# Optimization experiments

Measured on AMD Instinct MI355X. Metric: run time of the kernel, lower is better.

Reference implementation:

```python
import jax, jax.numpy as jnp
import numpy as np

N_HEADS = 32
N_KV_HEADS = 8
HEAD_DIM = 64
D_MODEL = 2048
SLIDING_WINDOW = 512
ROPE_THETA = 10000.0
PAST_LENGTH = 0
EPS = 1e-6


def setup_inputs() -> dict:
    key = jax.random.key(0)
    k1, k2, k3 = jax.random.split(key, 3)
    B, S = 1, 2048
    q_size = N_HEADS * HEAD_DIM
    kv_size = N_KV_HEADS * HEAD_DIM
    return {
        "x": jax.random.normal(k1, (B, S, D_MODEL), dtype=jnp.float32),
        "w_qkv": jax.random.normal(k2, (q_size + 2 * kv_size, D_MODEL), dtype=jnp.float32) * (D_MODEL ** -0.5),
        "w_out": jax.random.normal(k3, (D_MODEL, q_size), dtype=jnp.float32) * (q_size ** -0.5),
        "q_norm_w": jnp.ones((HEAD_DIM,), dtype=jnp.float32),
        "k_norm_w": jnp.ones((HEAD_DIM,), dtype=jnp.float32),
    }


def _rms_norm(x, w):
    xf = x.astype(jnp.float32)
    rms = jax.lax.rsqrt(jnp.mean(xf * xf, axis=-1, keepdims=True) + EPS)
    return (xf * rms).astype(x.dtype) * w


def _rope(q, k, past_length):
    # q: [b, h, s, d], k: [b, kv, s, d]
    s, d = q.shape[2], q.shape[3]
    inv_freq = 1.0 / (ROPE_THETA ** (jnp.arange(0, d, 2, dtype=jnp.float32) / d))
    pos = jnp.arange(s, dtype=jnp.float32) + past_length
    ang = pos[:, None] * inv_freq[None, :]            # [s, d/2]
    emb = jnp.concatenate([ang, ang], axis=-1)        # [s, d]
    cos, sin = jnp.cos(emb), jnp.sin(emb)

    def rot_half(x):
        x1, x2 = jnp.split(x, 2, axis=-1)
        return jnp.concatenate([-x2, x1], axis=-1)

    q = q * cos + rot_half(q) * sin
    k = k * cos + rot_half(k) * sin
    return q, k


def _sliding_mask(seq_len, total_len, past_length):
    q_idx = jnp.arange(seq_len)[:, None]
    k_idx = jnp.arange(total_len)[None, :]
    causal = (q_idx + past_length) >= k_idx
    window = (q_idx + past_length - k_idx) < SLIDING_WINDOW
    keep = causal & window
    return jnp.where(keep, 0.0, -jnp.inf).astype(jnp.float32)[None, None]


def reference(x, w_qkv, w_out, q_norm_w, k_norm_w):
    b, s, _ = x.shape
    n_rep = N_HEADS // N_KV_HEADS
    q_size = N_HEADS * HEAD_DIM
    kv_size = N_KV_HEADS * HEAD_DIM

    qkv = jnp.einsum('bsd,od->bso', x, w_qkv)
    q, k, v = jnp.split(qkv, [q_size, q_size + kv_size], axis=-1)
    q = q.reshape(b, s, N_HEADS, HEAD_DIM).transpose(0, 2, 1, 3)
    k = k.reshape(b, s, N_KV_HEADS, HEAD_DIM).transpose(0, 2, 1, 3)
    v = v.reshape(b, s, N_KV_HEADS, HEAD_DIM).transpose(0, 2, 1, 3)

    q = _rms_norm(q, q_norm_w)
    k = _rms_norm(k, k_norm_w)
    q, k = _rope(q, k, PAST_LENGTH)

    k_rep = jnp.repeat(k, n_rep, axis=1)  # [b, H, s, d]
    v_rep = jnp.repeat(v, n_rep, axis=1)

    scale = HEAD_DIM ** -0.5
    scores = jnp.einsum('bhqd,bhkd->bhqk', q, k_rep) * scale
    scores = scores + _sliding_mask(s, s, PAST_LENGTH)
    probs = jax.nn.softmax(scores, axis=-1)
    attn = jnp.einsum('bhqk,bhkd->bhqd', probs, v_rep)

    attn = attn.transpose(0, 2, 1, 3).reshape(b, s, q_size)
    return jnp.einsum('bso,do->bsd', attn, w_out)
```

## Files before the change

### kernel.cpp

```cpp
#include <hip/hip_runtime.h>

typedef unsigned short u16;
typedef unsigned int u32;
typedef __bf16 bf16x8 __attribute__((ext_vector_type(8)));
typedef float f32x4 __attribute__((ext_vector_type(4)));
typedef float f32x16 __attribute__((ext_vector_type(16)));
typedef u16 u16x8 __attribute__((ext_vector_type(8)));
typedef u32 u32x2 __attribute__((ext_vector_type(2)));

#define MFMA16(a, b, c) __builtin_amdgcn_mfma_f32_16x16x32_bf16((a), (b), (c), 0, 0, 0)
#define MFMA32(a, b, c) __builtin_amdgcn_mfma_f32_32x32x16_bf16((a), (b), (c), 0, 0, 0)

__device__ __forceinline__ u16 f2bf(float f) {
    unsigned int u = __float_as_uint(f);
    u = (u + 0x7FFF + ((u >> 16) & 1)) >> 16;
    return (u16)u;
}

__device__ __forceinline__ u32 cvtpk(float a, float b) {
    u32 d;
    asm("v_cvt_pk_bf16_f32 %0, %1, %2" : "=v"(d) : "v"(a), "v"(b));
    return d;
}

__device__ __forceinline__ void gld_lds16(const u16* g, u16* l) {
    __builtin_amdgcn_global_load_lds(
        (const __attribute__((address_space(1))) unsigned int*)g,
        (__attribute__((address_space(3))) unsigned int*)l, 16, 0, 0);
}

__global__ __launch_bounds__(256) void cvt_bf16(const float* __restrict__ in,
                                                u16* __restrict__ out, int n4) {
    int idx = blockIdx.x * blockDim.x + threadIdx.x;
    int stride = gridDim.x * blockDim.x;
    for (int i = idx; i < n4; i += stride) {
        float4 v = reinterpret_cast<const float4*>(in)[i];
        ushort4 o;
        o.x = f2bf(v.x); o.y = f2bf(v.y); o.z = f2bf(v.z); o.w = f2bf(v.w);
        reinterpret_cast<ushort4*>(out)[i] = o;
    }
}

__global__ __launch_bounds__(256) void reduce_add(const float4* __restrict__ a,
                                                  const float4* __restrict__ b,
                                                  float4* __restrict__ o, int n4) {
    int idx = blockIdx.x * blockDim.x + threadIdx.x;
    int stride = gridDim.x * blockDim.x;
    for (int i = idx; i < n4; i += stride) {
        float4 va = a[i], vb = b[i];
        float4 vo = {va.x + vb.x, va.y + vb.y, va.z + vb.z, va.w + vb.w};
        o[i] = vo;
    }
}

template <int SPLITK>
__global__ __launch_bounds__(256) void gemm_bt(const u16* __restrict__ A,
                                               const u16* __restrict__ B,
                                               float* __restrict__ C,
                                               int M, int N, int K) {
    __shared__ __align__(16) u16 As[2][128 * 32];
    __shared__ __align__(16) u16 Bs[2][128 * 32];

    int nbn = N >> 7;
    int bid = blockIdx.x;
    int nwg = (M >> 7) * nbn;
    int cpx = nwg >> 3;
    int wg = (bid & 7) * cpx + (bid >> 3);
    int tm = wg / nbn, tn = wg % nbn;
    int m0 = tm << 7, n0 = tn << 7;

    int Ks = K / SPLITK;
    int kbase = blockIdx.y * Ks;
    float* Cs = C + (size_t)blockIdx.y * ((size_t)M * N);

    int t = threadIdx.x;
    int w = t >> 6, l = t & 63, lrow = l & 15, lhi = l >> 4;
    int wr = w >> 1, wc = w & 1;

    int e0 = t * 8;
    int row0 = e0 >> 5, col0 = e0 & 31;

    const u16* Ag = A + (size_t)m0 * K + kbase;
    const u16* Bg = B + (size_t)n0 * K + kbase;

    auto stage = [&](int sbuf, int kt) {
        int k0 = kt << 5;
        gld_lds16(Ag + (size_t)row0 * K + k0 + col0, &As[sbuf][e0]);
        gld_lds16(Ag + (size_t)(row0 + 64) * K + k0 + col0, &As[sbuf][e0 + 2048]);
        gld_lds16(Bg + (size_t)row0 * K + k0 + col0, &Bs[sbuf][e0]);
        gld_lds16(Bg + (size_t)(row0 + 64) * K + k0 + col0, &Bs[sbuf][e0 + 2048]);
    };

    f32x4 acc[4][4] = {};
    int NT = Ks >> 5;
    stage(0, 0);
    __syncthreads();
    int buf = 0;
    for (int kt = 0; kt < NT; ++kt) {
        if (kt + 1 < NT) stage(buf ^ 1, kt + 1);
        bf16x8 af[4], bfr[4];
#pragma unroll
        for (int i = 0; i < 4; ++i) {
            af[i]  = *(const bf16x8*)&As[buf][(wr * 64 + i * 16 + lrow) * 32 + lhi * 8];
            bfr[i] = *(const bf16x8*)&Bs[buf][(wc * 64 + i * 16 + lrow) * 32 + lhi * 8];
        }
#pragma unroll
        for (int i = 0; i < 4; ++i)
#pragma unroll
            for (int j = 0; j < 4; ++j)
                acc[i][j] = MFMA16(af[i], bfr[j], acc[i][j]);
        __syncthreads();
        buf ^= 1;
    }
#pragma unroll
    for (int i = 0; i < 4; ++i) {
#pragma unroll
        for (int j = 0; j < 4; ++j) {
            int crow = m0 + wr * 64 + i * 16 + lhi * 4;
            int ccol = n0 + wc * 64 + j * 16 + lrow;
            float* cp = Cs + (size_t)crow * N + ccol;
#pragma unroll
            for (int r2 = 0; r2 < 4; ++r2) cp[(size_t)r2 * N] = acc[i][j][r2];
        }
    }
}

__global__ __launch_bounds__(256) void qkv_post(const float* __restrict__ qkv0,
                                                const float* __restrict__ qkv1,
                                                const float* __restrict__ qw,
                                                const float* __restrict__ kw,
                                                u16* __restrict__ qb,
                                                u16* __restrict__ kb,
                                                u16* __restrict__ vb) {
    int s = blockIdx.x;
    int t = threadIdx.x, w = t >> 6, lane = t & 63;
    const float* row0 = qkv0 + (size_t)s * 3072;
    const float* row1 = qkv1 + (size_t)s * 3072;
    int d2 = lane & 31;
    float inv = exp2f(-(float)d2 * (13.287712379549449f / 32.0f));
    float ang = (float)s * inv;
    float cs = cosf(ang), sn = sinf(ang);
    for (int h = w; h < 48; h += 4) {
        float v = row0[h * 64 + lane] + row1[h * 64 + lane];
        if (h < 40) {
            float ss = v * v;
#pragma unroll
            for (int m = 32; m; m >>= 1) ss += __shfl_xor(ss, m);
            float rms = rsqrtf(ss * (1.0f / 64.0f) + 1e-6f);
            float wgt = (h < 32) ? qw[lane] : kw[lane];
            v = v * rms * wgt;
            float part = __shfl_xor(v, 32);
            float rot = (lane < 32) ? -part : part;
            v = v * cs + rot * sn;
            if (h < 32)
                qb[((size_t)h * 2048 + s) * 64 + lane] = f2bf(v);
            else
                kb[((size_t)(h - 32) * 2048 + s) * 64 + lane] = f2bf(v);
        } else {
            vb[((size_t)(h - 40) * 2048 + s) * 64 + lane] = f2bf(v);
        }
    }
}

__global__ __launch_bounds__(256) void transpose_v(const u16* __restrict__ vb,
                                                   u16* __restrict__ vt) {
    int kv = blockIdx.y;
    int s0 = blockIdx.x * 256;
    __shared__ __align__(16) u16 tile[64][256];
    int t = threadIdx.x;
    int sl = t >> 3;
    int d0 = (t & 7) * 8;
#pragma unroll
    for (int j = 0; j < 8; ++j) {
        int s = sl + j * 32;
        u16x8 v = *(const u16x8*)(vb + ((size_t)kv * 2048 + s0 + s) * 64 + d0);
#pragma unroll
        for (int e = 0; e < 8; ++e) tile[d0 + e][s] = v[e];
    }
    __syncthreads();
    int d = t >> 2;
    int so = (t & 3) * 64;
#pragma unroll
    for (int j = 0; j < 8; ++j) {
        int s_local = so + j * 8;
        *(u16x8*)(vt + ((size_t)kv * 64 + d) * 2048 + s0 + s_local) =
            *(const u16x8*)&tile[d][s_local];
    }
}

__global__ __launch_bounds__(256) void attn_fa2(const u16* __restrict__ qb,
                                                const u16* __restrict__ kb,
                                                const u16* __restrict__ vt,
                                                u16* __restrict__ ab) {
    const float C = 0.18033688011112042f;
    int h = blockIdx.y, kv = h >> 2;
    int t = threadIdx.x, w = t >> 6, l = t & 63;
    int lq = l & 31, hi = l >> 5;
    int qlo = blockIdx.x * 128 + w * 32;
    __shared__ u16 sm[4][32][66];

    const u16* qrow = qb + ((size_t)h * 2048 + qlo + lq) * 64 + hi * 8;
    bf16x8 qf[4];
#pragma unroll
    for (int dk = 0; dk < 4; ++dk) qf[dk] = *(const bf16x8*)(qrow + dk * 16);

    f32x16 oa = {}, ob = {};
    float m = 0.f, lsum = 0.f;

    int kstart = qlo - 511; if (kstart < 0) kstart = 0;
    int kt0 = kstart >> 5, kt1 = qlo >> 5;
    const u16* kb_h = kb + (size_t)kv * 2048 * 64;
    const u16* vt_h = vt + (size_t)kv * 64 * 2048;

    for (int kt = kt0; kt <= kt1; ++kt) {
        int k0 = kt << 5;
        const u16* krow = kb_h + (size_t)(k0 + lq) * 64 + hi * 8;
        bf16x8 kf0 = *(const bf16x8*)(krow);
        bf16x8 kf1 = *(const bf16x8*)(krow + 16);
        bf16x8 kf2 = *(const bf16x8*)(krow + 32);
        bf16x8 kf3 = *(const bf16x8*)(krow + 48);
        const u16* vrow = vt_h + (size_t)lq * 2048 + k0 + hi * 8;
        bf16x8 va0 = *(const bf16x8*)(vrow);
        bf16x8 va1 = *(const bf16x8*)(vrow + 16);
        bf16x8 vb0 = *(const bf16x8*)(vrow + 32 * 2048);
        bf16x8 vb1 = *(const bf16x8*)(vrow + 32 * 2048 + 16);

        f32x16 s = {};
        s = MFMA32(kf0, qf[0], s);
        s = MFMA32(kf1, qf[1], s);
        s = MFMA32(kf2, qf[2], s);
        s = MFMA32(kf3, qf[3], s);

        bool edge = (k0 + 31 > qlo) || (qlo + 31 - k0 >= 512);
        if (edge) {
            int q = qlo + lq;
#pragma unroll
            for (int r = 0; r < 16; ++r) {
                int k = k0 + (r & 3) + 8 * (r >> 2) + 4 * hi;
                if (!((unsigned)(q - k) < 512u)) s[r] = -1e30f;
            }
        }
        float tm = s[0];
#pragma unroll
        for (int r = 1; r < 16; ++r) tm = fmaxf(tm, s[r]);
        tm = fmaxf(tm, __shfl_xor(tm, 32));
        float mnew = fmaxf(m, tm);
        float mc = mnew * C;
        float sf = exp2f(m * C - mc);
        m = mnew;
        float p[16];
        float rs = 0.f;
#pragma unroll
        for (int r = 0; r < 16; ++r) {
            p[r] = exp2f(fmaf(s[r], C, -mc));
            rs += p[r];
        }
        rs += __shfl_xor(rs, 32);
        lsum = lsum * sf + rs;
#pragma unroll
        for (int r = 0; r < 16; ++r) { oa[r] *= sf; ob[r] *= sf; }

        u32 pk0 = cvtpk(p[0], p[1]),   pk1 = cvtpk(p[2], p[3]);
        u32 pk2 = cvtpk(p[4], p[5]),   pk3 = cvtpk(p[6], p[7]);
        u32 pk4 = cvtpk(p[8], p[9]),   pk5 = cvtpk(p[10], p[11]);
        u32 pk6 = cvtpk(p[12], p[13]), pk7 = cvtpk(p[14], p[15]);
        u32x2 r02 = __builtin_amdgcn_permlane32_swap(pk0, pk2, false, false);
        u32x2 r13 = __builtin_amdgcn_permlane32_swap(pk1, pk3, false, false);
        u32x2 r46 = __builtin_amdgcn_permlane32_swap(pk4, pk6, false, false);
        u32x2 r57 = __builtin_amdgcn_permlane32_swap(pk5, pk7, false, false);
        bf16x8 b0, b1;
        {
            u32* bp = (u32*)&b0;
            bp[0] = r02[0]; bp[1] = r13[0]; bp[2] = r02[1]; bp[3] = r13[1];
            u32* bq = (u32*)&b1;
            bq[0] = r46[0]; bq[1] = r57[0]; bq[2] = r46[1]; bq[3] = r57[1];
        }
        oa = MFMA32(va0, b0, oa);
        oa = MFMA32(va1, b1, oa);
        ob = MFMA32(vb0, b0, ob);
        ob = MFMA32(vb1, b1, ob);
    }

    float inv = 1.0f / lsum;
#pragma unroll
    for (int rp = 0; rp < 8; ++rp) {
        int r = rp * 2;
        int d = (r & 3) + 8 * (r >> 2) + 4 * hi;
        *(u32*)&sm[w][lq][d]      = cvtpk(oa[r] * inv, oa[r + 1] * inv);
        *(u32*)&sm[w][lq][d + 32] = cvtpk(ob[r] * inv, ob[r + 1] * inv);
    }
    asm volatile("s_waitcnt lgkmcnt(0)" ::: "memory");
    int qr = l >> 1, dbase = (l & 1) * 32;
    size_t orow = (size_t)(qlo + qr) * 2048 + h * 64 + dbase;
#pragma unroll
    for (int c2 = 0; c2 < 8; ++c2) {
        u32 w0 = *(const u32*)&sm[w][qr][dbase + c2 * 4];
        u32 w1 = *(const u32*)&sm[w][qr][dbase + c2 * 4 + 2];
        u32x2 val = { w0, w1 };
        *(u32x2*)(ab + orow + c2 * 4) = val;
    }
}

extern "C" void kernel_launch(void* const* d_in, const int* in_sizes, int n_in,
                              void* d_out, int out_size, void* d_ws, size_t ws_size,
                              hipStream_t stream) {
    const float* x     = (const float*)d_in[0];
    const float* w_qkv = (const float*)d_in[1];
    const float* w_out = (const float*)d_in[2];
    const float* qw    = (const float*)d_in[3];
    const float* kw    = (const float*)d_in[4];
    float* out = (float*)d_out;

    char* ws = (char*)d_ws;
    u16*   x_b    = (u16*)(ws);
    u16*   wB     = (u16*)(ws + 8388608);
    u16*   q_b    = (u16*)(ws);
    u16*   k_b    = (u16*)(ws + 8388608);
    u16*   v_b    = (u16*)(ws + 10485760);
    u16*   v_t    = (u16*)(ws + 12582912);
    float* P0     = (float*)(ws + 20971520);
    float* O0     = (float*)(ws + 20971520);
    float* O1     = (float*)(ws + 37748736);
    u16*   attn_b = (u16*)(ws + 54525952);

    cvt_bf16<<<2048, 256, 0, stream>>>(x, x_b, 2048 * 2048 / 4);
    cvt_bf16<<<2048, 256, 0, stream>>>(w_qkv, wB, 3072 * 2048 / 4);
    gemm_bt<2><<<dim3(384, 2), 256, 0, stream>>>(x_b, wB, P0, 2048, 3072, 2048);
    qkv_post<<<2048, 256, 0, stream>>>(P0, P0 + (size_t)2048 * 3072, qw, kw, q_b, k_b, v_b);
    transpose_v<<<dim3(8, 8), 256, 0, stream>>>(v_b, v_t);
    attn_fa2<<<dim3(16, 32), 256, 0, stream>>>(q_b, k_b, v_t, attn_b);
    cvt_bf16<<<2048, 256, 0, stream>>>(w_out, wB, 2048 * 2048 / 4);
    gemm_bt<2><<<dim3(256, 2), 256, 0, stream>>>(attn_b, wB, O0, 2048, 2048, 2048);
    reduce_add<<<1024, 256, 0, stream>>>((const float4*)O0, (const float4*)O1,
                                         (float4*)out, 2048 * 2048 / 4);
}
```

Before: 145.6 us.

## Split sliding-window key tiles across waves and merge partial softmax in LDS

Each attention block now handles 32 queries instead of 128. Its four waves take interleaved key tiles of that window, and the grid grows from 512 to 2048 blocks. At the end, each wave writes its unnormalised output, running max and running sum to shared memory. After a barrier the block rescales and merges the four partial softmax states, then writes bf16 output with 16-byte stores. This shortens the serial per-wave loop over key tiles and adds parallelism, at the cost of a block-wide sync, extra fp32 LDS traffic and merge arithmetic. Each block also reloads the Q fragments redundantly.

```diff
diff --git a/kernel.cpp b/kernel.cpp
--- a/kernel.cpp
+++ b/kernel.cpp
@@ -7,6 +7,7 @@
 typedef float f32x16 __attribute__((ext_vector_type(16)));
 typedef u16 u16x8 __attribute__((ext_vector_type(8)));
 typedef u32 u32x2 __attribute__((ext_vector_type(2)));
+typedef u32 u32x4 __attribute__((ext_vector_type(4)));
 
 #define MFMA16(a, b, c) __builtin_amdgcn_mfma_f32_16x16x32_bf16((a), (b), (c), 0, 0, 0)
 #define MFMA32(a, b, c) __builtin_amdgcn_mfma_f32_32x32x16_bf16((a), (b), (c), 0, 0, 0)
@@ -188,7 +189,7 @@
     }
 }
 
-__global__ __launch_bounds__(256) void attn_fa2(const u16* __restrict__ qb,
+__global__ __launch_bounds__(256) void attn_fa3(const u16* __restrict__ qb,
                                                 const u16* __restrict__ kb,
                                                 const u16* __restrict__ vt,
                                                 u16* __restrict__ ab) {
@@ -196,8 +197,9 @@
     int h = blockIdx.y, kv = h >> 2;
     int t = threadIdx.x, w = t >> 6, l = t & 63;
     int lq = l & 31, hi = l >> 5;
-    int qlo = blockIdx.x * 128 + w * 32;
-    __shared__ u16 sm[4][32][66];
+    int qlo = blockIdx.x * 32;
+    __shared__ float Olds[4][64][32];
+    __shared__ float mlds[4][32], llds[4][32];
 
     const u16* qrow = qb + ((size_t)h * 2048 + qlo + lq) * 64 + hi * 8;
     bf16x8 qf[4];
@@ -212,7 +214,7 @@
     const u16* kb_h = kb + (size_t)kv * 2048 * 64;
     const u16* vt_h = vt + (size_t)kv * 64 * 2048;
 
-    for (int kt = kt0; kt <= kt1; ++kt) {
+    for (int kt = kt0 + w; kt <= kt1; kt += 4) {
         int k0 = kt << 5;
         const u16* krow = kb_h + (size_t)(k0 + lq) * 64 + hi * 8;
         bf16x8 kf0 = *(const bf16x8*)(krow);
@@ -281,24 +283,32 @@
         ob = MFMA32(vb1, b1, ob);
     }
 
-    float inv = 1.0f / lsum;
-#pragma unroll
-    for (int rp = 0; rp < 8; ++rp) {
-        int r = rp * 2;
+#pragma unroll
+    for (int r = 0; r < 16; ++r) {
         int d = (r & 3) + 8 * (r >> 2) + 4 * hi;
-        *(u32*)&sm[w][lq][d]      = cvtpk(oa[r] * inv, oa[r + 1] * inv);
-        *(u32*)&sm[w][lq][d + 32] = cvtpk(ob[r] * inv, ob[r + 1] * inv);
-    }
-    asm volatile("s_waitcnt lgkmcnt(0)" ::: "memory");
-    int qr = l >> 1, dbase = (l & 1) * 32;
-    size_t orow = (size_t)(qlo + qr) * 2048 + h * 64 + dbase;
-#pragma unroll
-    for (int c2 = 0; c2 < 8; ++c2) {
-        u32 w0 = *(const u32*)&sm[w][qr][dbase + c2 * 4];
-        u32 w1 = *(const u32*)&sm[w][qr][dbase + c2 * 4 + 2];
-        u32x2 val = { w0, w1 };
-        *(u32x2*)(ab + orow + c2 * 4) = val;
-    }
+        Olds[w][d][lq]      = oa[r];
+        Olds[w][d + 32][lq] = ob[r];
+    }
+    if (hi == 0) { mlds[w][lq] = m; llds[w][lq] = lsum; }
+    __syncthreads();
+
+    int q = t & 31, dg = t >> 5;
+    float m0 = mlds[0][q], m1 = mlds[1][q], m2 = mlds[2][q], m3 = mlds[3][q];
+    float M = fmaxf(fmaxf(m0, m1), fmaxf(m2, m3));
+    float s0 = exp2f((m0 - M) * C), s1 = exp2f((m1 - M) * C);
+    float s2 = exp2f((m2 - M) * C), s3 = exp2f((m3 - M) * C);
+    float lt = llds[0][q] * s0 + llds[1][q] * s1 + llds[2][q] * s2 + llds[3][q] * s3;
+    float inv = 1.0f / lt;
+    float v[8];
+#pragma unroll
+    for (int e = 0; e < 8; ++e) {
+        int d = dg * 8 + e;
+        v[e] = (Olds[0][d][q] * s0 + Olds[1][d][q] * s1 +
+                Olds[2][d][q] * s2 + Olds[3][d][q] * s3) * inv;
+    }
+    u32x4 pkt = { cvtpk(v[0], v[1]), cvtpk(v[2], v[3]),
+                  cvtpk(v[4], v[5]), cvtpk(v[6], v[7]) };
+    *(u32x4*)(ab + (size_t)(qlo + q) * 2048 + h * 64 + dg * 8) = pkt;
 }
 
 extern "C" void kernel_launch(void* const* d_in, const int* in_sizes, int n_in,
@@ -328,7 +338,7 @@
     gemm_bt<2><<<dim3(384, 2), 256, 0, stream>>>(x_b, wB, P0, 2048, 3072, 2048);
     qkv_post<<<2048, 256, 0, stream>>>(P0, P0 + (size_t)2048 * 3072, qw, kw, q_b, k_b, v_b);
     transpose_v<<<dim3(8, 8), 256, 0, stream>>>(v_b, v_t);
-    attn_fa2<<<dim3(16, 32), 256, 0, stream>>>(q_b, k_b, v_t, attn_b);
+    attn_fa3<<<dim3(64, 32), 256, 0, stream>>>(q_b, k_b, v_t, attn_b);
     cvt_bf16<<<2048, 256, 0, stream>>>(w_out, wB, 2048 * 2048 / 4);
     gemm_bt<2><<<dim3(256, 2), 256, 0, stream>>>(attn_b, wB, O0, 2048, 2048, 2048);
     reduce_add<<<1024, 256, 0, stream>>>((const float4*)O0, (const float4*)O1,
```

Measured after the change: 148.0 us. No clear change (+1.6%).

## Triple-buffer GEMM with swizzled LDS; stage K/V in LDS and drop online-softmax max

Applied to the files above, without the earlier changes.

The GEMM moves from double to triple buffering, prefetching three k-tiles ahead with explicit vmcnt waits and barriers. It also XOR-swizzles the LDS tile layout to avoid bank conflicts on the fragment reads. The attention kernel now loads each K/V tile cooperatively into double-buffered, swizzled LDS shared by all four waves, instead of every wave reading global memory. It also folds the softmax scale into Q and drops the running-max rescaling, relying on RMS-normalised Q/K keeping the logits bounded. That last step removes per-tile max/shuffle/rescale work but can overflow if the norm weights are large, and waves with no work still have to join every barrier.

```diff
diff --git a/kernel.cpp b/kernel.cpp
--- a/kernel.cpp
+++ b/kernel.cpp
@@ -7,6 +7,7 @@
 typedef float f32x16 __attribute__((ext_vector_type(16)));
 typedef u16 u16x8 __attribute__((ext_vector_type(8)));
 typedef u32 u32x2 __attribute__((ext_vector_type(2)));
+typedef u32 u32x4 __attribute__((ext_vector_type(4)));
 
 #define MFMA16(a, b, c) __builtin_amdgcn_mfma_f32_16x16x32_bf16((a), (b), (c), 0, 0, 0)
 #define MFMA32(a, b, c) __builtin_amdgcn_mfma_f32_32x32x16_bf16((a), (b), (c), 0, 0, 0)
@@ -58,8 +59,8 @@
                                                const u16* __restrict__ B,
                                                float* __restrict__ C,
                                                int M, int N, int K) {
-    __shared__ __align__(16) u16 As[2][128 * 32];
-    __shared__ __align__(16) u16 Bs[2][128 * 32];
+    __shared__ __align__(16) u16 As[3][128 * 32];
+    __shared__ __align__(16) u16 Bs[3][128 * 32];
 
     int nbn = N >> 7;
     int bid = blockIdx.x;
@@ -78,7 +79,8 @@
     int wr = w >> 1, wc = w & 1;
 
     int e0 = t * 8;
-    int row0 = e0 >> 5, col0 = e0 & 31;
+    int row0 = t >> 2;
+    int col0 = (((t & 3) ^ ((t >> 3) & 3)) << 3);
 
     const u16* Ag = A + (size_t)m0 * K + kbase;
     const u16* Bg = B + (size_t)n0 * K + kbase;
@@ -93,24 +95,38 @@
 
     f32x4 acc[4][4] = {};
     int NT = Ks >> 5;
-    stage(0, 0);
-    __syncthreads();
-    int buf = 0;
+    stage(0, 0); stage(1, 1); stage(2, 2);
+    asm volatile("s_waitcnt vmcnt(8)" ::: "memory");
+    asm volatile("s_barrier" ::: "memory");
+    int cur = 0;
     for (int kt = 0; kt < NT; ++kt) {
-        if (kt + 1 < NT) stage(buf ^ 1, kt + 1);
         bf16x8 af[4], bfr[4];
 #pragma unroll
         for (int i = 0; i < 4; ++i) {
-            af[i]  = *(const bf16x8*)&As[buf][(wr * 64 + i * 16 + lrow) * 32 + lhi * 8];
-            bfr[i] = *(const bf16x8*)&Bs[buf][(wc * 64 + i * 16 + lrow) * 32 + lhi * 8];
-        }
+            int row = wr * 64 + i * 16 + lrow;
+            af[i] = *(const bf16x8*)&As[cur][row * 32 + ((lhi ^ ((row >> 1) & 3)) << 3)];
+        }
+#pragma unroll
+        for (int j = 0; j < 4; ++j) {
+            int row = wc * 64 + j * 16 + lrow;
+            bfr[j] = *(const bf16x8*)&Bs[cur][row * 32 + ((lhi ^ ((row >> 1) & 3)) << 3)];
+        }
+        asm volatile("s_waitcnt lgkmcnt(0)" ::: "memory");
+        __builtin_amdgcn_sched_barrier(0);
+        asm volatile("s_barrier" ::: "memory");
+        if (kt + 3 < NT) stage(cur, kt + 3);
 #pragma unroll
         for (int i = 0; i < 4; ++i)
 #pragma unroll
             for (int j = 0; j < 4; ++j)
                 acc[i][j] = MFMA16(af[i], bfr[j], acc[i][j]);
-        __syncthreads();
-        buf ^= 1;
+        if (kt + 1 < NT) {
+            if (kt + 3 < NT)      asm volatile("s_waitcnt vmcnt(8)" ::: "memory");
+            else if (kt + 2 < NT) asm volatile("s_waitcnt vmcnt(4)" ::: "memory");
+            else                  asm volatile("s_waitcnt vmcnt(0)" ::: "memory");
+            asm volatile("s_barrier" ::: "memory");
+        }
+        cur = (cur == 2) ? 0 : cur + 1;
     }
 #pragma unroll
     for (int i = 0; i < 4; ++i) {
@@ -132,6 +148,7 @@
                                                 u16* __restrict__ qb,
                                                 u16* __restrict__ kb,
                                                 u16* __restrict__ vb) {
+    const float C = 0.18033688011112042f;
     int s = blockIdx.x;
     int t = threadIdx.x, w = t >> 6, lane = t & 63;
     const float* row0 = qkv0 + (size_t)s * 3072;
@@ -153,7 +170,7 @@
             float rot = (lane < 32) ? -part : part;
             v = v * cs + rot * sn;
             if (h < 32)
-                qb[((size_t)h * 2048 + s) * 64 + lane] = f2bf(v);
+                qb[((size_t)h * 2048 + s) * 64 + lane] = f2bf(v * C);
             else
                 kb[((size_t)(h - 32) * 2048 + s) * 64 + lane] = f2bf(v);
         } else {
@@ -188,15 +205,17 @@
     }
 }
 
-__global__ __launch_bounds__(256) void attn_fa2(const u16* __restrict__ qb,
+__global__ __launch_bounds__(256) void attn_fa7(const u16* __restrict__ qb,
                                                 const u16* __restrict__ kb,
                                                 const u16* __restrict__ vt,
                                                 u16* __restrict__ ab) {
-    const float C = 0.18033688011112042f;
-    int h = blockIdx.y, kv = h >> 2;
+    int qt = blockIdx.x, h = blockIdx.y, kv = h >> 2;
     int t = threadIdx.x, w = t >> 6, l = t & 63;
     int lq = l & 31, hi = l >> 5;
-    int qlo = blockIdx.x * 128 + w * 32;
+    int qlo_blk = qt * 128;
+    int qlo = qlo_blk + w * 32;
+    __shared__ __align__(16) u16 Kt[2][32 * 64];
+    __shared__ __align__(16) u16 Vt[2][64 * 32];
     __shared__ u16 sm[4][32][66];
 
     const u16* qrow = qb + ((size_t)h * 2048 + qlo + lq) * 64 + hi * 8;
@@ -205,82 +224,95 @@
     for (int dk = 0; dk < 4; ++dk) qf[dk] = *(const bf16x8*)(qrow + dk * 16);
 
     f32x16 oa = {}, ob = {};
-    float m = 0.f, lsum = 0.f;
-
-    int kstart = qlo - 511; if (kstart < 0) kstart = 0;
-    int kt0 = kstart >> 5, kt1 = qlo >> 5;
+    float lsum = 0.f;
+
+    int ktA = (qlo_blk >= 512) ? ((qlo_blk >> 5) - 16) : 0;
+    int ktB = (qlo_blk >> 5) + 3;
     const u16* kb_h = kb + (size_t)kv * 2048 * 64;
     const u16* vt_h = vt + (size_t)kv * 64 * 2048;
 
-    for (int kt = kt0; kt <= kt1; ++kt) {
+    int sk_row = t >> 3, sk_c = ((t & 7) ^ (sk_row & 7)) << 3;
+    int sv_row = t >> 2, sv_c = (((t & 3) ^ ((t >> 3) & 3))) << 3;
+
+    auto stage = [&](int buf, int kt) {
         int k0 = kt << 5;
-        const u16* krow = kb_h + (size_t)(k0 + lq) * 64 + hi * 8;
-        bf16x8 kf0 = *(const bf16x8*)(krow);
-        bf16x8 kf1 = *(const bf16x8*)(krow + 16);
-        bf16x8 kf2 = *(const bf16x8*)(krow + 32);
-        bf16x8 kf3 = *(const bf16x8*)(krow + 48);
-        const u16* vrow = vt_h + (size_t)lq * 2048 + k0 + hi * 8;
-        bf16x8 va0 = *(const bf16x8*)(vrow);
-        bf16x8 va1 = *(const bf16x8*)(vrow + 16);
-        bf16x8 vb0 = *(const bf16x8*)(vrow + 32 * 2048);
-        bf16x8 vb1 = *(const bf16x8*)(vrow + 32 * 2048 + 16);
-
-        f32x16 s = {};
-        s = MFMA32(kf0, qf[0], s);
-        s = MFMA32(kf1, qf[1], s);
-        s = MFMA32(kf2, qf[2], s);
-        s = MFMA32(kf3, qf[3], s);
-
-        bool edge = (k0 + 31 > qlo) || (qlo + 31 - k0 >= 512);
-        if (edge) {
-            int q = qlo + lq;
+        gld_lds16(kb_h + (size_t)(k0 + sk_row) * 64 + sk_c, &Kt[buf][t * 8]);
+        gld_lds16(vt_h + (size_t)sv_row * 2048 + k0 + sv_c, &Vt[buf][t * 8]);
+    };
+
+    stage(0, ktA);
+    int cur = 0;
+    for (int kt = ktA; kt <= ktB; ++kt) {
+        if (kt < ktB) {
+            stage(cur ^ 1, kt + 1);
+            asm volatile("s_waitcnt vmcnt(2)" ::: "memory");
+        } else {
+            asm volatile("s_waitcnt vmcnt(0)" ::: "memory");
+        }
+        asm volatile("s_barrier" ::: "memory");
+
+        int k0 = kt << 5;
+        bool active = (k0 <= qlo + 31) && (k0 >= qlo - 542);
+        if (active) {
+            bf16x8 kf[4], vaf[2], vbf[2];
+#pragma unroll
+            for (int c = 0; c < 4; ++c)
+                kf[c] = *(const bf16x8*)&Kt[cur][lq * 64 + (((c * 2 + hi) ^ (lq & 7)) << 3)];
+#pragma unroll
+            for (int vi = 0; vi < 2; ++vi) {
+                int swz = ((vi * 2 + hi) ^ ((lq >> 1) & 3)) << 3;
+                vaf[vi] = *(const bf16x8*)&Vt[cur][lq * 32 + swz];
+                vbf[vi] = *(const bf16x8*)&Vt[cur][(lq + 32) * 32 + swz];
+            }
+            asm volatile("s_waitcnt lgkmcnt(0)" ::: "memory");
+            __builtin_amdgcn_sched_barrier(0);
+
+            f32x16 s = {};
+            s = MFMA32(kf[0], qf[0], s);
+            s = MFMA32(kf[1], qf[1], s);
+            s = MFMA32(kf[2], qf[2], s);
+            s = MFMA32(kf[3], qf[3], s);
+
+            bool edge = (k0 + 31 > qlo) || (qlo + 31 - k0 >= 512);
+            if (edge) {
+                int q = qlo + lq;
+#pragma unroll
+                for (int r = 0; r < 16; ++r) {
+                    int k = k0 + (r & 3) + 8 * (r >> 2) + 4 * hi;
+                    if (!((unsigned)(q - k) < 512u)) s[r] = -1e30f;
+                }
+            }
+            float p[16];
 #pragma unroll
             for (int r = 0; r < 16; ++r) {
-                int k = k0 + (r & 3) + 8 * (r >> 2) + 4 * hi;
-                if (!((unsigned)(q - k) < 512u)) s[r] = -1e30f;
+                p[r] = exp2f(s[r]);
+                lsum += p[r];
             }
-        }
-        float tm = s[0];
-#pragma unroll
-        for (int r = 1; r < 16; ++r) tm = fmaxf(tm, s[r]);
-        tm = fmaxf(tm, __shfl_xor(tm, 32));
-        float mnew = fmaxf(m, tm);
-        float mc = mnew * C;
-        float sf = exp2f(m * C - mc);
-        m = mnew;
-        float p[16];
-        float rs = 0.f;
-#pragma unroll
-        for (int r = 0; r < 16; ++r) {
-            p[r] = exp2f(fmaf(s[r], C, -mc));
-            rs += p[r];
-        }
-        rs += __shfl_xor(rs, 32);
-        lsum = lsum * sf + rs;
-#pragma unroll
-        for (int r = 0; r < 16; ++r) { oa[r] *= sf; ob[r] *= sf; }
-
-        u32 pk0 = cvtpk(p[0], p[1]),   pk1 = cvtpk(p[2], p[3]);
-        u32 pk2 = cvtpk(p[4], p[5]),   pk3 = cvtpk(p[6], p[7]);
-        u32 pk4 = cvtpk(p[8], p[9]),   pk5 = cvtpk(p[10], p[11]);
-        u32 pk6 = cvtpk(p[12], p[13]), pk7 = cvtpk(p[14], p[15]);
-        u32x2 r02 = __builtin_amdgcn_permlane32_swap(pk0, pk2, false, false);
-        u32x2 r13 = __builtin_amdgcn_permlane32_swap(pk1, pk3, false, false);
-        u32x2 r46 = __builtin_amdgcn_permlane32_swap(pk4, pk6, false, false);
-        u32x2 r57 = __builtin_amdgcn_permlane32_swap(pk5, pk7, false, false);
-        bf16x8 b0, b1;
-        {
-            u32* bp = (u32*)&b0;
-            bp[0] = r02[0]; bp[1] = r13[0]; bp[2] = r02[1]; bp[3] = r13[1];
-            u32* bq = (u32*)&b1;
-            bq[0] = r46[0]; bq[1] = r57[0]; bq[2] = r46[1]; bq[3] = r57[1];
-        }
-        oa = MFMA32(va0, b0, oa);
-        oa = MFMA32(va1, b1, oa);
-        ob = MFMA32(vb0, b0, ob);
-        ob = MFMA32(vb1, b1, ob);
-    }
-
+            u32 pk0 = cvtpk(p[0], p[1]),   pk1 = cvtpk(p[2], p[3]);
+            u32 pk2 = cvtpk(p[4], p[5]),   pk3 = cvtpk(p[6], p[7]);
+            u32 pk4 = cvtpk(p[8], p[9]),   pk5 = cvtpk(p[10], p[11]);
+            u32 pk6 = cvtpk(p[12], p[13]), pk7 = cvtpk(p[14], p[15]);
+            u32x2 r02 = __builtin_amdgcn_permlane32_swap(pk0, pk2, false, false);
+            u32x2 r13 = __builtin_amdgcn_permlane32_swap(pk1, pk3, false, false);
+            u32x2 r46 = __builtin_amdgcn_permlane32_swap(pk4, pk6, false, false);
+            u32x2 r57 = __builtin_amdgcn_permlane32_swap(pk5, pk7, false, false);
+            bf16x8 b0, b1;
+            {
+                u32* bp = (u32*)&b0;
+                bp[0] = r02[0]; bp[1] = r13[0]; bp[2] = r02[1]; bp[3] = r13[1];
+                u32* bq = (u32*)&b1;
+                bq[0] = r46[0]; bq[1] = r57[0]; bq[2] = r46[1]; bq[3] = r57[1];
+            }
+            oa = MFMA32(vaf[0], b0, oa);
+            oa = MFMA32(vaf[1], b1, oa);
+            ob = MFMA32(vbf[0], b0, ob);
+            ob = MFMA32(vbf[1], b1, ob);
+        }
+        asm volatile("s_barrier" ::: "memory");
+        cur ^= 1;
+    }
+
+    lsum += __shfl_xor(lsum, 32);
     float inv = 1.0f / lsum;
 #pragma unroll
     for (int rp = 0; rp < 8; ++rp) {
@@ -328,7 +360,7 @@
     gemm_bt<2><<<dim3(384, 2), 256, 0, stream>>>(x_b, wB, P0, 2048, 3072, 2048);
     qkv_post<<<2048, 256, 0, stream>>>(P0, P0 + (size_t)2048 * 3072, qw, kw, q_b, k_b, v_b);
     transpose_v<<<dim3(8, 8), 256, 0, stream>>>(v_b, v_t);
-    attn_fa2<<<dim3(16, 32), 256, 0, stream>>>(q_b, k_b, v_t, attn_b);
+    attn_fa7<<<dim3(16, 32), 256, 0, stream>>>(q_b, k_b, v_t, attn_b);
     cvt_bf16<<<2048, 256, 0, stream>>>(w_out, wB, 2048 * 2048 / 4);
     gemm_bt<2><<<dim3(256, 2), 256, 0, stream>>>(attn_b, wB, O0, 2048, 2048, 2048);
     reduce_add<<<1024, 256, 0, stream>>>((const float4*)O0, (const float4*)O1,
```

Result: faster. 142.4 us (-2.2%).
